# Kernel optimization log

Measured on AMD Instinct MI355X. Metric: run time of the kernel, lower is better.

The kernel has to match this reference:

```python
import jax, jax.numpy as jnp
import numpy as np

T = 2048
HIDDEN = 4096
NQ = 32
NKV = 8
HD = 128
THETA = 10000.0


def setup_inputs() -> dict:
    key = jax.random.key(0)
    ks = jax.random.split(key, 5)
    s = 1.0 / np.sqrt(HIDDEN)
    return {
        "positions": jnp.arange(T, dtype=jnp.int32),
        "hidden_states": jax.random.normal(ks[0], (T, HIDDEN), dtype=jnp.float32),
        "wq": jax.random.normal(ks[1], (HIDDEN, NQ * HD), dtype=jnp.float32) * s,
        "wk": jax.random.normal(ks[2], (HIDDEN, NKV * HD), dtype=jnp.float32) * s,
        "wv": jax.random.normal(ks[3], (HIDDEN, NKV * HD), dtype=jnp.float32) * s,
        "wo": jax.random.normal(ks[4], (NQ * HD, HIDDEN), dtype=jnp.float32) * s,
    }


def _rope_neox(x, positions):
    # x: [T, H, HD]; neox style: split halves, rotate
    half = HD // 2
    inv_freq = 1.0 / (THETA ** (jnp.arange(0, half, dtype=jnp.float32) / half))
    ang = positions.astype(jnp.float32)[:, None] * inv_freq[None, :]  # [T, half]
    cos = jnp.cos(ang)[:, None, :]  # [T, 1, half]
    sin = jnp.sin(ang)[:, None, :]
    x1, x2 = x[..., :half], x[..., half:]
    return jnp.concatenate([x1 * cos - x2 * sin, x2 * cos + x1 * sin], axis=-1)


def reference(positions, hidden_states, wq, wk, wv, wo):
    scale = HD ** -0.5
    q = (hidden_states @ wq).reshape(T, NQ, HD)
    k = (hidden_states @ wk).reshape(T, NKV, HD)
    v = (hidden_states @ wv).reshape(T, NKV, HD)
    q = _rope_neox(q, positions)
    k = _rope_neox(k, positions)
    # GQA: repeat kv heads to match q heads
    group = NQ // NKV
    k_r = jnp.repeat(k, group, axis=1)  # [T, NQ, HD]
    v_r = jnp.repeat(v, group, axis=1)
    scores = jnp.einsum('qhd,khd->hqk', q, k_r) * scale  # [NQ, T, T]
    causal = positions[:, None] >= positions[None, :]  # [T, T]
    scores = jnp.where(causal[None, :, :], scores, -jnp.inf)
    probs = jax.nn.softmax(scores, axis=-1)
    attn = jnp.einsum('hqk,khd->qhd', probs, v_r).reshape(T, NQ * HD)
    return attn @ wo
```

## Files before the change

kernel.cpp:

```cpp
#include <hip/hip_runtime.h>

#define T_SEQ  2048
#define HID    4096
#define NQH    32
#define NKVH   8
#define HDIM   128

typedef float  f32x4  __attribute__((ext_vector_type(4)));
typedef __bf16 bf16x8 __attribute__((ext_vector_type(8)));

__device__ __forceinline__ float bf2f(unsigned short u) {
  union { unsigned int i; float f; } v; v.i = ((unsigned int)u) << 16; return v.f;
}
__device__ __forceinline__ unsigned short f2bf(float f) {
  union { float f; unsigned int i; } v; v.f = f;
  unsigned int r = v.i + 0x7fffu + ((v.i >> 16) & 1u);
  return (unsigned short)(r >> 16);
}

__device__ __forceinline__ f32x4 mfma_bf16(bf16x8 a, bf16x8 b, f32x4 c) {
  return __builtin_amdgcn_mfma_f32_16x16x32_bf16(a, b, c, 0, 0, 0);
}

#define GLOAD16(g, l)                                              \
  __builtin_amdgcn_global_load_lds(                                \
      (const __attribute__((address_space(1))) void*)(g),          \
      (__attribute__((address_space(3))) void*)(l), 16, 0, 0)

__global__ void prep_qw(const float* __restrict__ hs, unsigned short* __restrict__ hb,
                        const float* __restrict__ wq, unsigned short* __restrict__ wt) {
  __shared__ float tile[64][65];
  if (blockIdx.x < 8192) {
    long long i = ((long long)blockIdx.x * 256 + threadIdx.x) * 4;
    float4 v = *(const float4*)(hs + i);
    union { unsigned short u[4]; uint2 p; } o;
    o.u[0] = f2bf(v.x); o.u[1] = f2bf(v.y); o.u[2] = f2bf(v.z); o.u[3] = f2bf(v.w);
    *(uint2*)(hb + i) = o.p;
    return;
  }
  const int bid = blockIdx.x - 8192;
  const int N = NQH * HDIM, K = HID;
  int n0 = (bid & 63) * 64, k0 = (bid >> 6) * 64;
  int tx = threadIdx.x & 15, ty = threadIdx.x >> 4;
#pragma unroll
  for (int i = 0; i < 4; i++) {
    int k = ty + 16 * i;
    float4 f = *(const float4*)(wq + (long long)(k0 + k) * N + n0 + tx * 4);
    tile[tx * 4 + 0][k] = f.x;
    tile[tx * 4 + 1][k] = f.y;
    tile[tx * 4 + 2][k] = f.z;
    tile[tx * 4 + 3][k] = f.w;
  }
  __syncthreads();
#pragma unroll
  for (int i = 0; i < 4; i++) {
    int n = ty + 16 * i;
    union { unsigned short u[4]; uint2 p; } o;
    o.u[0] = f2bf(tile[n][tx * 4 + 0]);
    o.u[1] = f2bf(tile[n][tx * 4 + 1]);
    o.u[2] = f2bf(tile[n][tx * 4 + 2]);
    o.u[3] = f2bf(tile[n][tx * 4 + 3]);
    *(uint2*)(wt + (long long)(n0 + n) * K + k0 + tx * 4) = o.p;
  }
}

__global__ void transpose_conv(const float* __restrict__ W,
                               unsigned short* __restrict__ Wt, int K, int N) {
  __shared__ float tile[64][65];
  int n0 = blockIdx.x * 64, k0 = blockIdx.y * 64;
  int tx = threadIdx.x & 15, ty = threadIdx.x >> 4;
#pragma unroll
  for (int i = 0; i < 4; i++) {
    int k = ty + 16 * i;
    float4 f = *(const float4*)(W + (long long)(k0 + k) * N + n0 + tx * 4);
    tile[tx * 4 + 0][k] = f.x;
    tile[tx * 4 + 1][k] = f.y;
    tile[tx * 4 + 2][k] = f.z;
    tile[tx * 4 + 3][k] = f.w;
  }
  __syncthreads();
#pragma unroll
  for (int i = 0; i < 4; i++) {
    int n = ty + 16 * i;
    union { unsigned short u[4]; uint2 p; } o;
    o.u[0] = f2bf(tile[n][tx * 4 + 0]);
    o.u[1] = f2bf(tile[n][tx * 4 + 1]);
    o.u[2] = f2bf(tile[n][tx * 4 + 2]);
    o.u[3] = f2bf(tile[n][tx * 4 + 3]);
    *(uint2*)(Wt + (long long)(n0 + n) * K + k0 + tx * 4) = o.p;
  }
}

__global__ void transpose_conv_kv(const float* __restrict__ Wk,
                                  const float* __restrict__ Wv,
                                  unsigned short* __restrict__ Wt) {
  __shared__ float tile[64][65];
  const int N = NKVH * HDIM, K = HID;
  const float* W = blockIdx.z ? Wv : Wk;
  unsigned short* dst = Wt + (size_t)blockIdx.z * N * K;
  int n0 = blockIdx.x * 64, k0 = blockIdx.y * 64;
  int tx = threadIdx.x & 15, ty = threadIdx.x >> 4;
#pragma unroll
  for (int i = 0; i < 4; i++) {
    int k = ty + 16 * i;
    float4 f = *(const float4*)(W + (long long)(k0 + k) * N + n0 + tx * 4);
    tile[tx * 4 + 0][k] = f.x;
    tile[tx * 4 + 1][k] = f.y;
    tile[tx * 4 + 2][k] = f.z;
    tile[tx * 4 + 3][k] = f.w;
  }
  __syncthreads();
#pragma unroll
  for (int i = 0; i < 4; i++) {
    int n = ty + 16 * i;
    union { unsigned short u[4]; uint2 p; } o;
    o.u[0] = f2bf(tile[n][tx * 4 + 0]);
    o.u[1] = f2bf(tile[n][tx * 4 + 1]);
    o.u[2] = f2bf(tile[n][tx * 4 + 2]);
    o.u[3] = f2bf(tile[n][tx * 4 + 3]);
    *(uint2*)(dst + (long long)(n0 + n) * K + k0 + tx * 4) = o.p;
  }
}

template <int EPI>
__global__ __launch_bounds__(256) void gemm_bt(const unsigned short* __restrict__ A,
                                               const unsigned short* __restrict__ Bt,
                                               void* __restrict__ Cv,
                                               int M, int N, int K) {
  __shared__ unsigned short As[128 * 64];
  __shared__ unsigned short Bs[128 * 64];
  const int lin = blockIdx.y * gridDim.x + blockIdx.x;
  const int cpx = (gridDim.x * gridDim.y) >> 3;
  const int swz = (lin & 7) * cpx + (lin >> 3);
  const int bx = swz % gridDim.x, by = swz / gridDim.x;

  const int t = threadIdx.x;
  const int lane = t & 63, w = t >> 6;
  const int wr = w >> 1, wc = w & 1;
  const int l15 = lane & 15, lg = lane >> 4;
  const int m0 = by * 128, n0 = bx * 128;

  f32x4 acc[4][4];
#pragma unroll
  for (int i = 0; i < 4; i++)
#pragma unroll
    for (int j = 0; j < 4; j++) acc[i][j] = (f32x4){0.f, 0.f, 0.f, 0.f};

  for (int kt = 0; kt < K; kt += 64) {
    __syncthreads();
#pragma unroll
    for (int s = 0; s < 4; s++) {
      int c = t + s * 256;
      int row = c >> 3, sub = c & 7;
      GLOAD16(A + (long long)(m0 + row) * K + kt + ((sub ^ (row & 7)) * 8),
              (char*)As + (w * 64 + s * 256) * 16);
      GLOAD16(Bt + (long long)(n0 + row) * K + kt + ((sub ^ (row & 7)) * 8),
              (char*)Bs + (w * 64 + s * 256) * 16);
    }
    __syncthreads();

#pragma unroll
    for (int kk = 0; kk < 2; kk++) {
      bf16x8 af[4], bfr[4];
#pragma unroll
      for (int mi = 0; mi < 4; mi++) {
        int row = wr * 64 + mi * 16 + l15;
        af[mi] = *(const bf16x8*)(As + row * 64 + (((kk * 4 + lg) ^ (row & 7)) * 8));
      }
#pragma unroll
      for (int ni = 0; ni < 4; ni++) {
        int row = wc * 64 + ni * 16 + l15;
        bfr[ni] = *(const bf16x8*)(Bs + row * 64 + (((kk * 4 + lg) ^ (row & 7)) * 8));
      }
#pragma unroll
      for (int mi = 0; mi < 4; mi++)
#pragma unroll
        for (int ni = 0; ni < 4; ni++)
          acc[mi][ni] = mfma_bf16(af[mi], bfr[ni], acc[mi][ni]);
    }
  }

  const int row0 = m0 + wr * 64, col0 = n0 + wc * 64;
#pragma unroll
  for (int mi = 0; mi < 4; mi++)
#pragma unroll
    for (int ni = 0; ni < 4; ni++) {
      int rbase = row0 + mi * 16 + lg * 4;
      int col = col0 + ni * 16 + l15;
#pragma unroll
      for (int r = 0; r < 4; r++) {
        float v = acc[mi][ni][r];
        if (EPI == 0)
          ((unsigned short*)Cv)[(long long)(rbase + r) * N + col] = f2bf(v);
        else
          ((float*)Cv)[(long long)(rbase + r) * N + col] = v;
      }
    }
}

__global__ __launch_bounds__(256) void gemm_kv64(const unsigned short* __restrict__ A,
                                                 const unsigned short* __restrict__ Bt,
                                                 unsigned short* __restrict__ Ckv,
                                                 unsigned short* __restrict__ Cvt) {
  __shared__ unsigned short As[64 * 64];
  __shared__ unsigned short Bs[128 * 64];
  __shared__ unsigned short Tt[128 * 64];
  const int lin = blockIdx.y * gridDim.x + blockIdx.x;
  const int swz = (lin & 7) * 64 + (lin >> 3);
  const int bx = swz & 15, by = swz >> 4;

  const int t = threadIdx.x;
  const int lane = t & 63, w = t >> 6;
  const int wr = w >> 1, wc = w & 1;
  const int l15 = lane & 15, lg = lane >> 4;
  const int m0 = by * 64, n0 = bx * 128;
  const int K = HID;

  f32x4 acc[2][4];
#pragma unroll
  for (int i = 0; i < 2; i++)
#pragma unroll
    for (int j = 0; j < 4; j++) acc[i][j] = (f32x4){0.f, 0.f, 0.f, 0.f};

  for (int kt = 0; kt < K; kt += 64) {
    __syncthreads();
#pragma unroll
    for (int s = 0; s < 2; s++) {
      int c = t + s * 256;
      int row = c >> 3, sub = c & 7;
      GLOAD16(A + (long long)(m0 + row) * K + kt + ((sub ^ (row & 7)) * 8),
              (char*)As + (w * 64 + s * 256) * 16);
    }
#pragma unroll
    for (int s = 0; s < 4; s++) {
      int c = t + s * 256;
      int row = c >> 3, sub = c & 7;
      GLOAD16(Bt + (long long)(n0 + row) * K + kt + ((sub ^ (row & 7)) * 8),
              (char*)Bs + (w * 64 + s * 256) * 16);
    }
    __syncthreads();

#pragma unroll
    for (int kk = 0; kk < 2; kk++) {
      bf16x8 af[2], bfr[4];
#pragma unroll
      for (int mi = 0; mi < 2; mi++) {
        int row = wr * 32 + mi * 16 + l15;
        af[mi] = *(const bf16x8*)(As + row * 64 + (((kk * 4 + lg) ^ (row & 7)) * 8));
      }
#pragma unroll
      for (int ni = 0; ni < 4; ni++) {
        int row = wc * 64 + ni * 16 + l15;
        bfr[ni] = *(const bf16x8*)(Bs + row * 64 + (((kk * 4 + lg) ^ (row & 7)) * 8));
      }
#pragma unroll
      for (int mi = 0; mi < 2; mi++)
#pragma unroll
        for (int ni = 0; ni < 4; ni++)
          acc[mi][ni] = mfma_bf16(af[mi], bfr[ni], acc[mi][ni]);
    }
  }

  const int row0 = m0 + wr * 32, col0 = n0 + wc * 64;
  if (n0 < 1024) {
#pragma unroll
    for (int mi = 0; mi < 2; mi++)
#pragma unroll
      for (int ni = 0; ni < 4; ni++) {
        int rbase = row0 + mi * 16 + lg * 4;
        int col = col0 + ni * 16 + l15;
#pragma unroll
        for (int r = 0; r < 4; r++)
          Ckv[(long long)(rbase + r) * 1024 + col] = f2bf(acc[mi][ni][r]);
      }
  } else {
#pragma unroll
    for (int mi = 0; mi < 2; mi++)
#pragma unroll
      for (int ni = 0; ni < 4; ni++) {
        int nloc = wc * 64 + ni * 16 + l15;
#pragma unroll
        for (int r = 0; r < 4; r++) {
          int mloc = wr * 32 + mi * 16 + lg * 4 + r;
          Tt[nloc * 64 + (mloc ^ ((nloc & 7) << 3))] = f2bf(acc[mi][ni][r]);
        }
      }
    __syncthreads();
    const int nloc = t >> 1;
#pragma unroll
    for (int cc = 0; cc < 8; cc++) {
      int ci = (t & 1) * 8 + cc;
      uint2 v = *(const uint2*)(Tt + nloc * 64 +
                                (((ci >> 1) ^ (nloc & 7)) * 8 + (ci & 1) * 4));
      int nc = (ci >> 3) * 8 + 2 * (ci & 3) + ((ci >> 2) & 1);
      *(uint2*)(Cvt + (long long)(n0 - 1024 + nloc) * T_SEQ + m0 + nc * 4) = v;
    }
  }
}

__global__ void rope_all(unsigned short* __restrict__ qb,
                         unsigned short* __restrict__ kb,
                         const int* __restrict__ positions,
                         int* __restrict__ cnt) {
  if (blockIdx.x == 0 && threadIdx.x < 8) cnt[threadIdx.x] = 0;
  const int w = threadIdx.x >> 6, d = threadIdx.x & 63;
  const int gid = blockIdx.x * 4 + w;
  unsigned short* row;
  int t;
  bool isq;
  if (gid < T_SEQ * NQH) {
    int h = gid & (NQH - 1); t = gid >> 5;
    row = qb + (size_t)t * (NQH * HDIM) + (size_t)h * HDIM;
    isq = true;
  } else {
    int g = gid - T_SEQ * NQH;
    int h = g & (NKVH - 1); t = g >> 3;
    row = kb + (size_t)t * (NKVH * HDIM) + (size_t)h * HDIM;
    isq = false;
  }
  double inv = exp2(-(double)d * 0.20762050593046014);
  double ang = (double)positions[t] * inv;
  double c = cos(ang), s = sin(ang);
  if (isq) { c *= 0.12751744416986895; s *= 0.12751744416986895; }
  float x1 = bf2f(row[d]), x2 = bf2f(row[d + 64]);
  row[d]      = f2bf((float)((double)x1 * c - (double)x2 * s));
  row[d + 64] = f2bf((float)((double)x2 * c + (double)x1 * s));
}

__global__ __launch_bounds__(256) void attn_kernel(const unsigned short* __restrict__ qb,
                                                   const unsigned short* __restrict__ kb,
                                                   const unsigned short* __restrict__ vt,
                                                   unsigned short* __restrict__ ab,
                                                   int* __restrict__ cnt) {
  __shared__ unsigned short Ks[64 * 128];
  __shared__ unsigned short Vs[128 * 64];
  __shared__ int s_item;

  const int xcd = blockIdx.x & 7;
  const int kvh = xcd;
  const int t = threadIdx.x, lane = t & 63, w = t >> 6;
  const int l15 = lane & 15, lg = lane >> 4;

  for (;;) {
    __syncthreads();
    if (t == 0) s_item = atomicAdd(&cnt[xcd], 1);
    __syncthreads();
    const int item = s_item;
    if (item >= 128) break;
    const int j = 31 - (item >> 2);
    const int head = xcd * 4 + (item & 3);
    const int q0 = j * 64;

    bf16x8 qf[4];
#pragma unroll
    for (int kk = 0; kk < 4; kk++)
      qf[kk] = *(const bf16x8*)(qb + (long long)(q0 + w * 16 + l15) * (NQH * HDIM) +
                                head * HDIM + kk * 32 + lg * 8);

    f32x4 accO[8];
#pragma unroll
    for (int db = 0; db < 8; db++) accO[db] = (f32x4){0.f, 0.f, 0.f, 0.f};
    float mrun = -3e38f, lrun = 0.f;

    for (int kt = 0; kt <= j; kt++) {
      __syncthreads();
#pragma unroll
      for (int s = 0; s < 4; s++) {
        int c = t + s * 256;
        int row = c >> 4, chk = c & 15;
        GLOAD16(kb + (long long)(kt * 64 + row) * (NKVH * HDIM) + kvh * HDIM +
                    ((chk ^ (row & 7)) * 8),
                (char*)Ks + (w * 64 + s * 256) * 16);
      }
#pragma unroll
      for (int s = 0; s < 4; s++) {
        int c = t + s * 256;
        int row = c >> 3, chk = c & 7;
        GLOAD16(vt + (long long)(kvh * HDIM + row) * T_SEQ + kt * 64 +
                    ((chk ^ (row & 7)) * 8),
                (char*)Vs + (w * 64 + s * 256) * 16);
      }
      __syncthreads();

      f32x4 accS[4];
#pragma unroll
      for (int kc = 0; kc < 4; kc++) accS[kc] = (f32x4){0.f, 0.f, 0.f, 0.f};
      __builtin_amdgcn_s_setprio(1);
#pragma unroll
      for (int kk = 0; kk < 4; kk++)
#pragma unroll
        for (int kc = 0; kc < 4; kc++) {
          int row = kc * 16 + l15;
          bf16x8 a = *(const bf16x8*)(Ks + row * 128 + (((kk * 4 + lg) ^ (l15 & 7)) * 8));
          accS[kc] = mfma_bf16(a, qf[kk], accS[kc]);
        }
      __builtin_amdgcn_s_setprio(0);

      float pm[4][4];
      if (kt == j) {
        const int qloc = w * 16 + l15;
#pragma unroll
        for (int kc = 0; kc < 4; kc++)
#pragma unroll
          for (int r = 0; r < 4; r++)
            pm[kc][r] = (kc * 16 + lg * 4 + r > qloc) ? -3e38f : accS[kc][r];
      } else {
#pragma unroll
        for (int kc = 0; kc < 4; kc++)
#pragma unroll
          for (int r = 0; r < 4; r++) pm[kc][r] = accS[kc][r];
      }

      float rm = pm[0][0];
#pragma unroll
      for (int kc = 0; kc < 4; kc++)
#pragma unroll
        for (int r = 0; r < 4; r++) rm = fmaxf(rm, pm[kc][r]);
      if (__any(rm > mrun + 8.f)) {
        rm = fmaxf(rm, __shfl_xor(rm, 16, 64));
        rm = fmaxf(rm, __shfl_xor(rm, 32, 64));
        float mn = fmaxf(mrun, rm);
        float corr = exp2f(mrun - mn);
        mrun = mn;
        lrun *= corr;
        float cO[4];
#pragma unroll
        for (int r = 0; r < 4; r++) cO[r] = __shfl(corr, lg * 4 + r, 64);
#pragma unroll
        for (int db = 0; db < 8; db++)
#pragma unroll
          for (int r = 0; r < 4; r++) accO[db][r] *= cO[r];
      }

      float p[4][4];
#pragma unroll
      for (int kc = 0; kc < 4; kc++)
#pragma unroll
        for (int r = 0; r < 4; r++) {
          p[kc][r] = exp2f(pm[kc][r] - mrun);
          lrun += p[kc][r];
        }
      bf16x8 pa0, pa1;
#pragma unroll
      for (int jj = 0; jj < 8; jj++) {
        pa0[jj] = (__bf16)p[(jj >> 2)][jj & 3];
        pa1[jj] = (__bf16)p[2 + (jj >> 2)][jj & 3];
      }

      __builtin_amdgcn_s_setprio(1);
#pragma unroll
      for (int db = 0; db < 8; db++) {
        int vrow = db * 16 + l15;
        bf16x8 b = *(const bf16x8*)(Vs + vrow * 64 + ((lg ^ (vrow & 7)) * 8));
        accO[db] = mfma_bf16(pa0, b, accO[db]);
      }
#pragma unroll
      for (int db = 0; db < 8; db++) {
        int vrow = db * 16 + l15;
        bf16x8 b = *(const bf16x8*)(Vs + vrow * 64 + (((4 + lg) ^ (vrow & 7)) * 8));
        accO[db] = mfma_bf16(pa1, b, accO[db]);
      }
      __builtin_amdgcn_s_setprio(0);
    }

    lrun += __shfl_xor(lrun, 16, 64);
    lrun += __shfl_xor(lrun, 32, 64);
    float lO[4];
#pragma unroll
    for (int r = 0; r < 4; r++) lO[r] = __shfl(lrun, lg * 4 + r, 64);
#pragma unroll
    for (int db = 0; db < 8; db++)
#pragma unroll
      for (int r = 0; r < 4; r++) {
        int qr = q0 + w * 16 + lg * 4 + r;
        int col = head * HDIM + db * 16 + l15;
        ((__bf16*)ab)[(long long)qr * (NQH * HDIM) + col] = (__bf16)(accO[db][r] / lO[r]);
      }
  }
}

extern "C" void kernel_launch(void* const* d_in, const int* in_sizes, int n_in,
                              void* d_out, int out_size, void* d_ws, size_t ws_size,
                              hipStream_t stream) {
  const int*   positions = (const int*)d_in[0];
  const float* hs = (const float*)d_in[1];
  const float* wq = (const float*)d_in[2];
  const float* wk = (const float*)d_in[3];
  const float* wv = (const float*)d_in[4];
  const float* wo = (const float*)d_in[5];
  float* out = (float*)d_out;

  const size_t SZ_WT = (size_t)HID * HID * 2;
  const size_t SZ_HB = (size_t)T_SEQ * HID * 2;
  const size_t SZ_QB = (size_t)T_SEQ * NQH * HDIM * 2;
  const size_t SZ_KB = (size_t)T_SEQ * NKVH * HDIM * 2;
  const size_t need = SZ_WT + SZ_HB + SZ_QB + SZ_KB * 2 + 64;
  if (ws_size < need) return;

  char* p = (char*)d_ws;
  unsigned short* wt  = (unsigned short*)p; p += SZ_WT;
  unsigned short* hb  = (unsigned short*)p; p += SZ_HB;
  unsigned short* qb  = (unsigned short*)p; p += SZ_QB;
  unsigned short* kb  = (unsigned short*)p; p += SZ_KB;
  unsigned short* vtb = (unsigned short*)p; p += SZ_KB;
  int* cnt = (int*)p;
  unsigned short* ab  = hb;

  prep_qw<<<8192 + 4096, 256, 0, stream>>>(hs, hb, wq, wt);
  gemm_bt<0><<<dim3((NQH * HDIM) / 128, T_SEQ / 128), 256, 0, stream>>>(hb, wt, qb, T_SEQ, NQH * HDIM, HID);

  transpose_conv_kv<<<dim3((NKVH * HDIM) / 64, HID / 64, 2), 256, 0, stream>>>(wk, wv, wt);
  gemm_kv64<<<dim3(16, 32), 256, 0, stream>>>(hb, wt, kb, vtb);

  rope_all<<<(T_SEQ * (NQH + NKVH)) / 4, 256, 0, stream>>>(qb, kb, positions, cnt);

  attn_kernel<<<512, 256, 0, stream>>>(qb, kb, vtb, ab, cnt);

  transpose_conv<<<dim3(HID / 64, (NQH * HDIM) / 64), 256, 0, stream>>>(wo, wt, NQH * HDIM, HID);
  gemm_bt<2><<<dim3(HID / 128, T_SEQ / 128), 256, 0, stream>>>(ab, wt, out, T_SEQ, HID, NQH * HDIM);
}
```

Measured before the change: 358.9 us.

## Fuse Q/K/V weight prep and projections into single launches

Merges the Wk/Wv transpose-convert into the hidden-state and Wq prep kernel, and replaces the separate Q GEMM and 64-row KV GEMM with one 128x128-tile GEMM over a 48x16 grid covering Q, K and V columns. The epilogue routes each tile to the Q buffer, the K buffer, or the transposed V buffer through an LDS transpose. This removes two launches and the kernel boundary tail between them, and gives the KV part larger tiles. In exchange it needs a separate workspace region for the KV weights and a larger V transpose tile in LDS.

```diff
diff --git a/kernel.cpp b/kernel.cpp
--- a/kernel.cpp
+++ b/kernel.cpp
@@ -27,25 +27,38 @@
       (const __attribute__((address_space(1))) void*)(g),          \
       (__attribute__((address_space(3))) void*)(l), 16, 0, 0)
 
-__global__ void prep_qw(const float* __restrict__ hs, unsigned short* __restrict__ hb,
-                        const float* __restrict__ wq, unsigned short* __restrict__ wt) {
+__global__ void prep_all(const float* __restrict__ hs, unsigned short* __restrict__ hb,
+                         const float* __restrict__ wq, unsigned short* __restrict__ wqt,
+                         const float* __restrict__ wk, const float* __restrict__ wv,
+                         unsigned short* __restrict__ wkvt) {
   __shared__ float tile[64][65];
-  if (blockIdx.x < 8192) {
-    long long i = ((long long)blockIdx.x * 256 + threadIdx.x) * 4;
+  const int b = blockIdx.x;
+  if (b < 8192) {
+    long long i = ((long long)b * 256 + threadIdx.x) * 4;
     float4 v = *(const float4*)(hs + i);
     union { unsigned short u[4]; uint2 p; } o;
     o.u[0] = f2bf(v.x); o.u[1] = f2bf(v.y); o.u[2] = f2bf(v.z); o.u[3] = f2bf(v.w);
     *(uint2*)(hb + i) = o.p;
     return;
   }
-  const int bid = blockIdx.x - 8192;
-  const int N = NQH * HDIM, K = HID;
-  int n0 = (bid & 63) * 64, k0 = (bid >> 6) * 64;
+  const float* W;
+  unsigned short* dst;
+  int N, n0, k0;
+  if (b < 12288) {
+    int bid = b - 8192;  W = wq;  dst = wqt;  N = 4096;
+    n0 = (bid & 63) * 64; k0 = (bid >> 6) * 64;
+  } else if (b < 13312) {
+    int bid = b - 12288; W = wk;  dst = wkvt; N = 1024;
+    n0 = (bid & 15) * 64; k0 = (bid >> 4) * 64;
+  } else {
+    int bid = b - 13312; W = wv;  dst = wkvt + (size_t)1024 * HID; N = 1024;
+    n0 = (bid & 15) * 64; k0 = (bid >> 4) * 64;
+  }
   int tx = threadIdx.x & 15, ty = threadIdx.x >> 4;
 #pragma unroll
   for (int i = 0; i < 4; i++) {
     int k = ty + 16 * i;
-    float4 f = *(const float4*)(wq + (long long)(k0 + k) * N + n0 + tx * 4);
+    float4 f = *(const float4*)(W + (long long)(k0 + k) * N + n0 + tx * 4);
     tile[tx * 4 + 0][k] = f.x;
     tile[tx * 4 + 1][k] = f.y;
     tile[tx * 4 + 2][k] = f.z;
@@ -60,7 +73,7 @@
     o.u[1] = f2bf(tile[n][tx * 4 + 1]);
     o.u[2] = f2bf(tile[n][tx * 4 + 2]);
     o.u[3] = f2bf(tile[n][tx * 4 + 3]);
-    *(uint2*)(wt + (long long)(n0 + n) * K + k0 + tx * 4) = o.p;
+    *(uint2*)(dst + (long long)(n0 + n) * HID + k0 + tx * 4) = o.p;
   }
 }
 
@@ -88,37 +101,6 @@
     o.u[2] = f2bf(tile[n][tx * 4 + 2]);
     o.u[3] = f2bf(tile[n][tx * 4 + 3]);
     *(uint2*)(Wt + (long long)(n0 + n) * K + k0 + tx * 4) = o.p;
-  }
-}
-
-__global__ void transpose_conv_kv(const float* __restrict__ Wk,
-                                  const float* __restrict__ Wv,
-                                  unsigned short* __restrict__ Wt) {
-  __shared__ float tile[64][65];
-  const int N = NKVH * HDIM, K = HID;
-  const float* W = blockIdx.z ? Wv : Wk;
-  unsigned short* dst = Wt + (size_t)blockIdx.z * N * K;
-  int n0 = blockIdx.x * 64, k0 = blockIdx.y * 64;
-  int tx = threadIdx.x & 15, ty = threadIdx.x >> 4;
-#pragma unroll
-  for (int i = 0; i < 4; i++) {
-    int k = ty + 16 * i;
-    float4 f = *(const float4*)(W + (long long)(k0 + k) * N + n0 + tx * 4);
-    tile[tx * 4 + 0][k] = f.x;
-    tile[tx * 4 + 1][k] = f.y;
-    tile[tx * 4 + 2][k] = f.z;
-    tile[tx * 4 + 3][k] = f.w;
-  }
-  __syncthreads();
-#pragma unroll
-  for (int i = 0; i < 4; i++) {
-    int n = ty + 16 * i;
-    union { unsigned short u[4]; uint2 p; } o;
-    o.u[0] = f2bf(tile[n][tx * 4 + 0]);
-    o.u[1] = f2bf(tile[n][tx * 4 + 1]);
-    o.u[2] = f2bf(tile[n][tx * 4 + 2]);
-    o.u[3] = f2bf(tile[n][tx * 4 + 3]);
-    *(uint2*)(dst + (long long)(n0 + n) * K + k0 + tx * 4) = o.p;
   }
 }
 
@@ -198,54 +180,56 @@
     }
 }
 
-__global__ __launch_bounds__(256) void gemm_kv64(const unsigned short* __restrict__ A,
-                                                 const unsigned short* __restrict__ Bt,
-                                                 unsigned short* __restrict__ Ckv,
-                                                 unsigned short* __restrict__ Cvt) {
-  __shared__ unsigned short As[64 * 64];
-  __shared__ unsigned short Bs[128 * 64];
-  __shared__ unsigned short Tt[128 * 64];
+__global__ __launch_bounds__(256) void gemm_qkv(const unsigned short* __restrict__ A,
+                                                const unsigned short* __restrict__ wqt,
+                                                const unsigned short* __restrict__ wkvt,
+                                                unsigned short* __restrict__ qb,
+                                                unsigned short* __restrict__ kb,
+                                                unsigned short* __restrict__ vtb) {
+  __shared__ unsigned short S[2 * 128 * 64];
+  unsigned short* As = S;
+  unsigned short* Bs = S + 128 * 64;
+  const int K = HID;
+
   const int lin = blockIdx.y * gridDim.x + blockIdx.x;
-  const int swz = (lin & 7) * 64 + (lin >> 3);
-  const int bx = swz & 15, by = swz >> 4;
+  const int cpx = (gridDim.x * gridDim.y) >> 3;
+  const int swz = (lin & 7) * cpx + (lin >> 3);
+  const int bx = swz % gridDim.x, by = swz / gridDim.x;
 
   const int t = threadIdx.x;
   const int lane = t & 63, w = t >> 6;
   const int wr = w >> 1, wc = w & 1;
   const int l15 = lane & 15, lg = lane >> 4;
-  const int m0 = by * 64, n0 = bx * 128;
-  const int K = HID;
-
-  f32x4 acc[2][4];
-#pragma unroll
-  for (int i = 0; i < 2; i++)
+  const int m0 = by * 128, n0 = bx * 128;
+
+  const unsigned short* Brow = (n0 < 4096) ? (wqt + (long long)n0 * K)
+                                           : (wkvt + (long long)(n0 - 4096) * K);
+
+  f32x4 acc[4][4];
+#pragma unroll
+  for (int i = 0; i < 4; i++)
 #pragma unroll
     for (int j = 0; j < 4; j++) acc[i][j] = (f32x4){0.f, 0.f, 0.f, 0.f};
 
   for (int kt = 0; kt < K; kt += 64) {
     __syncthreads();
 #pragma unroll
-    for (int s = 0; s < 2; s++) {
+    for (int s = 0; s < 4; s++) {
       int c = t + s * 256;
       int row = c >> 3, sub = c & 7;
       GLOAD16(A + (long long)(m0 + row) * K + kt + ((sub ^ (row & 7)) * 8),
               (char*)As + (w * 64 + s * 256) * 16);
-    }
-#pragma unroll
-    for (int s = 0; s < 4; s++) {
-      int c = t + s * 256;
-      int row = c >> 3, sub = c & 7;
-      GLOAD16(Bt + (long long)(n0 + row) * K + kt + ((sub ^ (row & 7)) * 8),
+      GLOAD16(Brow + (long long)row * K + kt + ((sub ^ (row & 7)) * 8),
               (char*)Bs + (w * 64 + s * 256) * 16);
     }
     __syncthreads();
 
 #pragma unroll
     for (int kk = 0; kk < 2; kk++) {
-      bf16x8 af[2], bfr[4];
-#pragma unroll
-      for (int mi = 0; mi < 2; mi++) {
-        int row = wr * 32 + mi * 16 + l15;
+      bf16x8 af[4], bfr[4];
+#pragma unroll
+      for (int mi = 0; mi < 4; mi++) {
+        int row = wr * 64 + mi * 16 + l15;
         af[mi] = *(const bf16x8*)(As + row * 64 + (((kk * 4 + lg) ^ (row & 7)) * 8));
       }
 #pragma unroll
@@ -254,46 +238,61 @@
         bfr[ni] = *(const bf16x8*)(Bs + row * 64 + (((kk * 4 + lg) ^ (row & 7)) * 8));
       }
 #pragma unroll
-      for (int mi = 0; mi < 2; mi++)
+      for (int mi = 0; mi < 4; mi++)
 #pragma unroll
         for (int ni = 0; ni < 4; ni++)
           acc[mi][ni] = mfma_bf16(af[mi], bfr[ni], acc[mi][ni]);
     }
   }
 
-  const int row0 = m0 + wr * 32, col0 = n0 + wc * 64;
-  if (n0 < 1024) {
-#pragma unroll
-    for (int mi = 0; mi < 2; mi++)
+  const int row0 = m0 + wr * 64;
+  if (n0 < 4096) {
+#pragma unroll
+    for (int mi = 0; mi < 4; mi++)
 #pragma unroll
       for (int ni = 0; ni < 4; ni++) {
         int rbase = row0 + mi * 16 + lg * 4;
-        int col = col0 + ni * 16 + l15;
+        int col = n0 + wc * 64 + ni * 16 + l15;
 #pragma unroll
         for (int r = 0; r < 4; r++)
-          Ckv[(long long)(rbase + r) * 1024 + col] = f2bf(acc[mi][ni][r]);
+          qb[(long long)(rbase + r) * 4096 + col] = f2bf(acc[mi][ni][r]);
+      }
+  } else if (n0 < 5120) {
+#pragma unroll
+    for (int mi = 0; mi < 4; mi++)
+#pragma unroll
+      for (int ni = 0; ni < 4; ni++) {
+        int rbase = row0 + mi * 16 + lg * 4;
+        int col = (n0 - 4096) + wc * 64 + ni * 16 + l15;
+#pragma unroll
+        for (int r = 0; r < 4; r++)
+          kb[(long long)(rbase + r) * 1024 + col] = f2bf(acc[mi][ni][r]);
       }
   } else {
-#pragma unroll
-    for (int mi = 0; mi < 2; mi++)
+    __syncthreads();
+    unsigned short* Tt = S;
+#pragma unroll
+    for (int mi = 0; mi < 4; mi++)
 #pragma unroll
       for (int ni = 0; ni < 4; ni++) {
         int nloc = wc * 64 + ni * 16 + l15;
 #pragma unroll
         for (int r = 0; r < 4; r++) {
-          int mloc = wr * 32 + mi * 16 + lg * 4 + r;
-          Tt[nloc * 64 + (mloc ^ ((nloc & 7) << 3))] = f2bf(acc[mi][ni][r]);
+          int mloc = wr * 64 + mi * 16 + lg * 4 + r;
+          Tt[nloc * 128 + (mloc & 64) + ((mloc & 63) ^ ((nloc & 7) << 3))] =
+              f2bf(acc[mi][ni][r]);
         }
       }
     __syncthreads();
     const int nloc = t >> 1;
-#pragma unroll
-    for (int cc = 0; cc < 8; cc++) {
-      int ci = (t & 1) * 8 + cc;
-      uint2 v = *(const uint2*)(Tt + nloc * 64 +
+    const int half = t & 1;
+    const int d0 = n0 - 5120;
+#pragma unroll
+    for (int ci = 0; ci < 16; ci++) {
+      uint2 v = *(const uint2*)(Tt + nloc * 128 + half * 64 +
                                 (((ci >> 1) ^ (nloc & 7)) * 8 + (ci & 1) * 4));
       int nc = (ci >> 3) * 8 + 2 * (ci & 3) + ((ci >> 2) & 1);
-      *(uint2*)(Cvt + (long long)(n0 - 1024 + nloc) * T_SEQ + m0 + nc * 4) = v;
+      *(uint2*)(vtb + (long long)(d0 + nloc) * T_SEQ + m0 + half * 64 + nc * 4) = v;
     }
   }
 }
@@ -490,32 +489,32 @@
   const float* wo = (const float*)d_in[5];
   float* out = (float*)d_out;
 
-  const size_t SZ_WT = (size_t)HID * HID * 2;
-  const size_t SZ_HB = (size_t)T_SEQ * HID * 2;
-  const size_t SZ_QB = (size_t)T_SEQ * NQH * HDIM * 2;
-  const size_t SZ_KB = (size_t)T_SEQ * NKVH * HDIM * 2;
-  const size_t need = SZ_WT + SZ_HB + SZ_QB + SZ_KB * 2 + 64;
+  const size_t SZ_WQT = (size_t)HID * HID * 2;
+  const size_t SZ_WKV = (size_t)2048 * HID * 2;
+  const size_t SZ_HB  = (size_t)T_SEQ * HID * 2;
+  const size_t SZ_QB  = (size_t)T_SEQ * NQH * HDIM * 2;
+  const size_t SZ_KB  = (size_t)T_SEQ * NKVH * HDIM * 2;
+  const size_t need = SZ_WQT + SZ_WKV + SZ_HB + SZ_QB + SZ_KB * 2 + 64;
   if (ws_size < need) return;
 
   char* p = (char*)d_ws;
-  unsigned short* wt  = (unsigned short*)p; p += SZ_WT;
-  unsigned short* hb  = (unsigned short*)p; p += SZ_HB;
-  unsigned short* qb  = (unsigned short*)p; p += SZ_QB;
-  unsigned short* kb  = (unsigned short*)p; p += SZ_KB;
-  unsigned short* vtb = (unsigned short*)p; p += SZ_KB;
+  unsigned short* wqt  = (unsigned short*)p; p += SZ_WQT;
+  unsigned short* wkvt = (unsigned short*)p; p += SZ_WKV;
+  unsigned short* hb   = (unsigned short*)p; p += SZ_HB;
+  unsigned short* qb   = (unsigned short*)p; p += SZ_QB;
+  unsigned short* kb   = (unsigned short*)p; p += SZ_KB;
+  unsigned short* vtb  = (unsigned short*)p; p += SZ_KB;
   int* cnt = (int*)p;
-  unsigned short* ab  = hb;
-
-  prep_qw<<<8192 + 4096, 256, 0, stream>>>(hs, hb, wq, wt);
-  gemm_bt<0><<<dim3((NQH * HDIM) / 128, T_SEQ / 128), 256, 0, stream>>>(hb, wt, qb, T_SEQ, NQH * HDIM, HID);
-
-  transpose_conv_kv<<<dim3((NKVH * HDIM) / 64, HID / 64, 2), 256, 0, stream>>>(wk, wv, wt);
-  gemm_kv64<<<dim3(16, 32), 256, 0, stream>>>(hb, wt, kb, vtb);
+  unsigned short* ab   = hb;
+
+  prep_all<<<14336, 256, 0, stream>>>(hs, hb, wq, wqt, wk, wv, wkvt);
+
+  gemm_qkv<<<dim3(48, 16), 256, 0, stream>>>(hb, wqt, wkvt, qb, kb, vtb);
 
   rope_all<<<(T_SEQ * (NQH + NKVH)) / 4, 256, 0, stream>>>(qb, kb, positions, cnt);
 
   attn_kernel<<<512, 256, 0, stream>>>(qb, kb, vtb, ab, cnt);
 
-  transpose_conv<<<dim3(HID / 64, (NQH * HDIM) / 64), 256, 0, stream>>>(wo, wt, NQH * HDIM, HID);
-  gemm_bt<2><<<dim3(HID / 128, T_SEQ / 128), 256, 0, stream>>>(ab, wt, out, T_SEQ, HID, NQH * HDIM);
-}
+  transpose_conv<<<dim3(HID / 64, (NQH * HDIM) / 64), 256, 0, stream>>>(wo, wqt, NQH * HDIM, HID);
+  gemm_bt<2><<<dim3(HID / 128, T_SEQ / 128), 256, 0, stream>>>(ab, wqt, out, T_SEQ, HID, NQH * HDIM);
+}
```

New measurement: 384.1 us. 7.0% more time.
